# Kernel optimization log

Measured on AMD Instinct MI355X. Metric: run time of the kernel, lower is better.

Reference implementation:

```python
import math
import jax, jax.numpy as jnp
import numpy as np

N_QUBITS = 16
BATCH = 128
N_STATE = 2 ** N_QUBITS


def cnot_ring(n_qubits):
    """Permutation equivalent to a CNOT ring (faithful copy of the torch repo's numpy code)."""
    n2 = np.array([0, 2, 3, 1])
    if n_qubits == 2:
        return n2
    evens = np.zeros(2 ** (n_qubits - 1))
    answer = n2[::2]
    for i in range(1, n_qubits - 1):
        evens[:2 ** i] = answer
        a, b = np.array_split(answer, 2)
        evens[2 ** i:2 ** i + 2 ** (i - 1)] = a + 3 * 2 ** i
        evens[2 ** i + 2 ** (i - 1):2 ** (i + 1)] = b + 2 ** i
        answer = evens[:2 ** (i + 1)]
    a, b = np.split(evens.copy() + 2 ** (n_qubits - 2), 2)
    a = np.mod(a, 2 ** (n_qubits - 1))
    b, c = np.split(b, 2)
    b = b - 2 ** (n_qubits - 1)
    odds = np.concatenate((a, b, c), axis=0)[::-1]
    output = np.zeros(2 ** n_qubits)
    output[::2] = evens
    output[1::2] = odds
    return output.astype(int)


def binary_mask(n_qubits):
    """[n, 2**n] matrix; row i is bit (n-1-i from LSB) of the column index,
    matching torch binary_matrix (dim 0 of the [2]*n tensor is the MSB)."""
    idx = jnp.arange(2 ** n_qubits, dtype=jnp.int32)
    shifts = (n_qubits - 1 - jnp.arange(n_qubits, dtype=jnp.int32))
    return ((idx[None, :] >> shifts[:, None]) & 1).astype(jnp.float32)


def wht(x):
    """Walsh-Hadamard transform over the last dim of [B, N] complex state (had_big butterfly)."""
    B, N = x.shape
    n = int(math.log2(N))
    for i in range(n):
        x = x.reshape(B, 2 ** i, 2, N >> (i + 1))
        a, b = x[:, :, 0, :], x[:, :, 1, :]
        x = jnp.stack([a + b, a - b], axis=2)
    return x.reshape(B, N) * jnp.asarray(2.0 ** (-n / 2), dtype=x.dtype)


def setup_inputs() -> dict:
    key = jax.random.key(0)
    k1, k2, k3 = jax.random.split(key, 3)
    state_re = jax.random.normal(k1, (BATCH, N_STATE), dtype=jnp.float32)
    state_im = jax.random.normal(k2, (BATCH, N_STATE), dtype=jnp.float32)
    thetas = jax.random.normal(k3, (BATCH, N_QUBITS), dtype=jnp.float32)
    cnot_p = jnp.asarray(cnot_ring(N_QUBITS), dtype=jnp.int32)
    return {"state_re": state_re, "state_im": state_im, "thetas": thetas, "cnot_p": cnot_p}


def reference(state_re, state_im, thetas, cnot_p):
    # set_state('random'): l2-normalize complex state per batch row
    norm = jnp.sqrt(jnp.sum(state_re * state_re + state_im * state_im, axis=-1, keepdims=True))
    state = (state_re + 1j * state_im) / norm  # complex64 [B, N]
    # hadamard layer (had_big WHT butterfly)
    state = wht(state)
    # RZ layer: thetas @ binary mask -> phase eigenvalues exp(-i*theta/2)
    ang = thetas @ binary_mask(N_QUBITS)  # [B, N]
    state = state * jnp.exp(-0.5j * ang)
    # CNOT ring: gather permutation over the state axis
    state = state[:, cnot_p]
    # second hadamard layer
    state = wht(state)
    # measure(): probabilities |psi|^2
    return jnp.abs(state) ** 2
```

## Files before the change

### kernel.cpp

```cpp
#include <hip/hip_runtime.h>

#define NB 128
#define NS 65536

typedef float v2f __attribute__((ext_vector_type(2)));

__device__ __forceinline__ v2f pk_fma(v2f a, v2f b, v2f c) {
  v2f d;
  asm("v_pk_fma_f32 %0, %1, %2, %3" : "=v"(d) : "v"(a), "v"(b), "v"(c));
  return d;
}
__device__ __forceinline__ v2f pk_add(v2f a, v2f b) {
  v2f d;
  asm("v_pk_add_f32 %0, %1, %2" : "=v"(d) : "v"(a), "v"(b));
  return d;
}
__device__ __forceinline__ v2f pk_mul(v2f a, v2f b) {
  v2f d;
  asm("v_pk_mul_f32 %0, %1, %2" : "=v"(d) : "v"(a), "v"(b));
  return d;
}

template <int CTRL>
__device__ __forceinline__ float dppmov(float x) {
  return __int_as_float(__builtin_amdgcn_update_dpp(
      0, __float_as_int(x), CTRL, 0xF, 0xF, false));
}
__device__ __forceinline__ float xor4mov(float x) {
  int t = __builtin_amdgcn_update_dpp(0, __float_as_int(x), 0x104, 0xF, 0x5, false);
  t = __builtin_amdgcn_update_dpp(t, __float_as_int(x), 0x114, 0xF, 0xA, false);
  return __int_as_float(t);
}

__device__ __forceinline__ void wht256p(v2f (&p)[4], int lane) {
  const v2f M1 = {-1.f, -1.f};
  {
    v2f t;
    t = p[0]; p[0] = pk_add(t, p[1]); p[1] = pk_fma(M1, p[1], t);
    t = p[2]; p[2] = pk_add(t, p[3]); p[3] = pk_fma(M1, p[3], t);
    t = p[0]; p[0] = pk_add(t, p[2]); p[2] = pk_fma(M1, p[2], t);
    t = p[1]; p[1] = pk_add(t, p[3]); p[3] = pk_fma(M1, p[3], t);
  }
  const float s1f  = (lane & 1)  ? -1.f : 1.f;
  const float s2f  = (lane & 2)  ? -1.f : 1.f;
  const float s4f  = (lane & 4)  ? -1.f : 1.f;
  const float s8f  = (lane & 8)  ? -1.f : 1.f;
  const float s16f = (lane & 16) ? -1.f : 1.f;
  const float s32f = (lane & 32) ? -1.f : 1.f;
  const v2f s1 = {s1f, s1f}, s2 = {s2f, s2f}, s4 = {s4f, s4f};
  const v2f s8 = {s8f, s8f}, s16 = {s16f, s16f}, s32 = {s32f, s32f};
#pragma unroll
  for (int q = 0; q < 4; ++q) {
    v2f m = {dppmov<0xB1>(p[q].x), dppmov<0xB1>(p[q].y)};
    p[q] = pk_fma(s1, p[q], m);
  }
#pragma unroll
  for (int q = 0; q < 4; ++q) {
    v2f m = {dppmov<0x4E>(p[q].x), dppmov<0x4E>(p[q].y)};
    p[q] = pk_fma(s2, p[q], m);
  }
#pragma unroll
  for (int q = 0; q < 4; ++q) {
    v2f m = {xor4mov(p[q].x), xor4mov(p[q].y)};
    p[q] = pk_fma(s4, p[q], m);
  }
#pragma unroll
  for (int q = 0; q < 4; ++q) {
    v2f m = {dppmov<0x128>(p[q].x), dppmov<0x128>(p[q].y)};
    p[q] = pk_fma(s8, p[q], m);
  }
#pragma unroll
  for (int q = 0; q < 4; ++q) {
    auto rre = __builtin_amdgcn_permlane16_swap(__float_as_uint(p[q].x),
                                                __float_as_uint(p[q].x), false, false);
    auto rim = __builtin_amdgcn_permlane16_swap(__float_as_uint(p[q].y),
                                                __float_as_uint(p[q].y), false, false);
    v2f lo = {__uint_as_float(rre[0]), __uint_as_float(rim[0])};
    v2f hi = {__uint_as_float(rre[1]), __uint_as_float(rim[1])};
    p[q] = pk_fma(s16, hi, lo);
  }
#pragma unroll
  for (int q = 0; q < 4; ++q) {
    auto rre = __builtin_amdgcn_permlane32_swap(__float_as_uint(p[q].x),
                                                __float_as_uint(p[q].x), false, false);
    auto rim = __builtin_amdgcn_permlane32_swap(__float_as_uint(p[q].y),
                                                __float_as_uint(p[q].y), false, false);
    v2f lo = {__uint_as_float(rre[0]), __uint_as_float(rim[0])};
    v2f hi = {__uint_as_float(rre[1]), __uint_as_float(rim[1])};
    p[q] = pk_fma(s32, hi, lo);
  }
}

__global__ __launch_bounds__(1024, 8) void k1_ahi(const float* __restrict__ sre,
                                                  const float* __restrict__ sim,
                                                  const float* __restrict__ thetas,
                                                  float* __restrict__ T,
                                                  float* __restrict__ partial) {
  __shared__ float sr[32][260];
  __shared__ float si[32][260];
  __shared__ float2 phh4[64];
  __shared__ float2 phHQ[4];
  __shared__ float red[16];
  const int bid = blockIdx.x;
  const int b = bid >> 3, tile = bid & 7;
  const int lo0 = tile * 32;
  const int tid = threadIdx.x, lane = tid & 63, w = tid >> 6;
  if (tid < 64) {
    const float* tb = thetas + b * 16;
    float a = 0.f;
#pragma unroll
    for (int i = 0; i < 6; ++i)
      if ((tid >> (5 - i)) & 1) a += tb[i];
    phh4[tid] = make_float2(cosf(0.5f * a), -sinf(0.5f * a));
    if (tid < 4) {
      float aq = 0.f;
      if (tid & 1) aq += tb[7];
      if (tid & 2) aq += tb[6];
      phHQ[tid] = make_float2(cosf(0.5f * aq), -sinf(0.5f * aq));
    }
  }
  const float* pre = sre + ((size_t)b << 16);
  const float* pim = sim + ((size_t)b << 16);
  const int c = tid & 7, jr = tid >> 3;
  const int j0 = jr, j1 = jr + 128;
  const float4 vr0 = *reinterpret_cast<const float4*>(pre + j0 * 256 + lo0 + c * 4);
  const float4 vi0 = *reinterpret_cast<const float4*>(pim + j0 * 256 + lo0 + c * 4);
  const float4 vr1 = *reinterpret_cast<const float4*>(pre + j1 * 256 + lo0 + c * 4);
  const float4 vi1 = *reinterpret_cast<const float4*>(pim + j1 * 256 + lo0 + c * 4);
  float acc = vr0.x*vr0.x + vr0.y*vr0.y + vr0.z*vr0.z + vr0.w*vr0.w
            + vi0.x*vi0.x + vi0.y*vi0.y + vi0.z*vi0.z + vi0.w*vi0.w
            + vr1.x*vr1.x + vr1.y*vr1.y + vr1.z*vr1.z + vr1.w*vr1.w
            + vi1.x*vi1.x + vi1.y*vi1.y + vi1.z*vi1.z + vi1.w*vi1.w;
  {
    const int fs = ((c >> 1) & 3) << 2;
    const int j0s = j0 ^ fs, j1s = j1 ^ fs;
    sr[c*4+0][j0s] = vr0.x; sr[c*4+1][j0s] = vr0.y; sr[c*4+2][j0s] = vr0.z; sr[c*4+3][j0s] = vr0.w;
    si[c*4+0][j0s] = vi0.x; si[c*4+1][j0s] = vi0.y; si[c*4+2][j0s] = vi0.z; si[c*4+3][j0s] = vi0.w;
    sr[c*4+0][j1s] = vr1.x; sr[c*4+1][j1s] = vr1.y; sr[c*4+2][j1s] = vr1.z; sr[c*4+3][j1s] = vr1.w;
    si[c*4+0][j1s] = vi1.x; si[c*4+1][j1s] = vi1.y; si[c*4+2][j1s] = vi1.z; si[c*4+3][j1s] = vi1.w;
  }
#pragma unroll
  for (int m = 32; m >= 1; m >>= 1) acc += __shfl_xor(acc, m, 64);
  if (lane == 0) red[w] = acc;
  __syncthreads();
  if (tid == 0) {
    float sm = 0.f;
#pragma unroll
    for (int k = 0; k < 16; ++k) sm += red[k];
    partial[bid] = sm;
  }
  const float2 p4 = phh4[lane];
  float prq[4], piq[4];
#pragma unroll
  for (int q = 0; q < 4; ++q) {
    const float2 pq = phHQ[q];
    prq[q] = p4.x * pq.x - p4.y * pq.y;
    piq[q] = p4.x * pq.y + p4.y * pq.x;
  }
#pragma unroll
  for (int r = 0; r < 2; ++r) {
    const int ll = w * 2 + r;
    const int blk = lane ^ ((ll >> 3) & 3);
    const float4 a4 = *reinterpret_cast<const float4*>(&sr[ll][blk * 4]);
    const float4 b4 = *reinterpret_cast<const float4*>(&si[ll][blk * 4]);
    v2f p[4] = {{a4.x, b4.x}, {a4.y, b4.y}, {a4.z, b4.z}, {a4.w, b4.w}};
    wht256p(p, lane);
#pragma unroll
    for (int q = 0; q < 4; ++q) {
      const float ur = p[q].x, ui = p[q].y;
      const v2f t = pk_mul(p[q], (v2f){prq[q], prq[q]});
      p[q].x = fmaf(-piq[q], ui, t.x);
      p[q].y = fmaf(piq[q], ur, t.y);
    }
    wht256p(p, lane);
    *reinterpret_cast<float4*>(&sr[ll][blk * 4]) =
        make_float4(p[0].x, p[1].x, p[2].x, p[3].x);
    *reinterpret_cast<float4*>(&si[ll][blk * 4]) =
        make_float4(p[0].y, p[1].y, p[2].y, p[3].y);
  }
  __syncthreads();
  float* Tb = T + ((size_t)b << 17);
  const int m = tid >> 2, sub = tid & 3;
  float* dst = Tb + ((size_t)m << 9) + (size_t)lo0 * 2;
#pragma unroll
  for (int j = 0; j < 4; ++j) {
    const int l0 = 8 * j + 2 * sub;
    const int ms = m ^ ((j & 3) << 2);
    *reinterpret_cast<float4*>(dst + l0 * 2) =
        make_float4(sr[l0][ms], si[l0][ms], sr[l0 + 1][ms], si[l0 + 1][ms]);
  }
}

__global__ __launch_bounds__(256, 8) void k2_alo_scatter(const float* __restrict__ T,
                                                         const float* __restrict__ thetas,
                                                         const int* __restrict__ cnot,
                                                         const float* __restrict__ partial,
                                                         float* __restrict__ outp) {
  __shared__ float2 phl4[64];
  __shared__ float2 phLQ[4];
  __shared__ int sloL[64];
  __shared__ int tj[16];
  __shared__ int srow16[16];
  __shared__ float th[16];
  __shared__ float shinv;
  const int bid = blockIdx.x;
  const int x = bid & 7, s2i = bid >> 3;
  const int b = x * 16 + (s2i >> 4), tile = s2i & 15;
  const int tid = threadIdx.x, lane = tid & 63, w = tid >> 6;
  if (tid < 16) {
    th[tid] = thetas[b * 16 + tid];
    int v = 0;
#pragma unroll
    for (int i = 0; i < 16; ++i) v |= ((cnot[1 << i] >> tid) & 1) << i;
    tj[tid] = v;
  }
  if (tid == 0) {
    float sum = 0.f;
#pragma unroll
    for (int k = 0; k < 8; ++k) sum += partial[b * 8 + k];
    shinv = 1.0f / (sum * 4294967296.0f);
  }
  __syncthreads();
  if (tid < 64) {
    float a = 0.f;
#pragma unroll
    for (int i = 0; i < 6; ++i)
      if ((tid >> (5 - i)) & 1) a += th[8 + i];
    phl4[tid] = make_float2(cosf(0.5f * a), -sinf(0.5f * a));
    int v = 0;
#pragma unroll
    for (int bb = 0; bb < 6; ++bb)
      if ((tid >> bb) & 1) v ^= tj[2 + bb];
    sloL[tid] = v;
    if (tid < 4) {
      float aq = 0.f;
      if (tid & 1) aq += th[15];
      if (tid & 2) aq += th[14];
      phLQ[tid] = make_float2(cosf(0.5f * aq), -sinf(0.5f * aq));
    }
  }
  if (tid < 16) {
    const int mh = tile * 16 + tid;
    int v = 0;
#pragma unroll
    for (int bb = 0; bb < 8; ++bb)
      if ((mh >> bb) & 1) v ^= tj[8 + bb];
    srow16[tid] = v;
  }
  __syncthreads();
  const float* Tb = T + ((size_t)b << 17);
  float* ob = outp + ((size_t)b << 16);
  const float iv = shinv;
  const float2 p4 = phl4[lane];
  const int sL = sloL[lane];
  const int sq1 = tj[0], sq2 = tj[1], sq3 = tj[0] ^ tj[1];
  float prq[4], piq[4];
#pragma unroll
  for (int q = 0; q < 4; ++q) {
    const float2 pq = phLQ[q];
    prq[q] = p4.x * pq.x - p4.y * pq.y;
    piq[q] = p4.x * pq.y + p4.y * pq.x;
  }
#pragma unroll
  for (int r = 0; r < 4; ++r) {
    const int rl = w * 4 + r;
    const int mh = tile * 16 + rl;
    const float4 va = *reinterpret_cast<const float4*>(Tb + ((size_t)mh << 9) + lane * 8);
    const float4 vb = *reinterpret_cast<const float4*>(Tb + ((size_t)mh << 9) + lane * 8 + 4);
    v2f p[4] = {{va.x, va.y}, {va.z, va.w}, {vb.x, vb.y}, {vb.z, vb.w}};
    wht256p(p, lane);
#pragma unroll
    for (int q = 0; q < 4; ++q) {
      const float ur = p[q].x, ui = p[q].y;
      const v2f t = pk_mul(p[q], (v2f){prq[q], prq[q]});
      p[q].x = fmaf(-piq[q], ui, t.x);
      p[q].y = fmaf(piq[q], ur, t.y);
    }
    wht256p(p, lane);
    const int base = srow16[rl] ^ sL;
    const v2f m0 = pk_mul(p[0], p[0]);
    const v2f m1 = pk_mul(p[1], p[1]);
    const v2f m2 = pk_mul(p[2], p[2]);
    const v2f m3 = pk_mul(p[3], p[3]);
    ob[base]       = (m0.x + m0.y) * iv;
    ob[base ^ sq1] = (m1.x + m1.y) * iv;
    ob[base ^ sq2] = (m2.x + m2.y) * iv;
    ob[base ^ sq3] = (m3.x + m3.y) * iv;
  }
}

extern "C" void kernel_launch(void* const* d_in, const int* in_sizes, int n_in,
                              void* d_out, int out_size, void* d_ws, size_t ws_size,
                              hipStream_t stream) {
  const float* sre = (const float*)d_in[0];
  const float* sim = (const float*)d_in[1];
  const float* thetas = (const float*)d_in[2];
  const int* cnot = (const int*)d_in[3];
  float* outp = (float*)d_out;
  char* w = (char*)d_ws;
  const size_t CPLANE = (size_t)NB * NS * 2 * sizeof(float);
  if (ws_size < CPLANE + 8192) return;
  float* T = (float*)(w);
  float* partial = (float*)(w + CPLANE);

  hipLaunchKernelGGL(k1_ahi, dim3(1024), dim3(1024), 0, stream, sre, sim, thetas, T, partial);
  hipLaunchKernelGGL(k2_alo_scatter, dim3(2048), dim3(256), 0, stream, T, thetas, cnot, partial, outp);
}
```

Measured before the change: 61.75 us.

## Fuse both passes into one kernel with per-batch atomic counter barrier

Merges the two kernels into a single launch of 512 blocks, four per batch row. Each block runs the first WHT/phase/WHT pass over two column tiles, publishes its partial norm, then spins on a per-batch atomic counter until all four blocks of that row have finished. It then runs the second pass and the CNOT scatter on its quarter of the rows. The aim is to drop the inter-kernel launch gap and let the intermediate buffer be read back while it is likely still in cache. The cost is an extra memset launch, less parallelism in the first pass, and a deadlock risk if the blocks of one batch are not all resident at the same time.

```diff
diff --git a/kernel.cpp b/kernel.cpp
--- a/kernel.cpp
+++ b/kernel.cpp
@@ -91,180 +91,166 @@
   }
 }
 
-__global__ __launch_bounds__(1024, 8) void k1_ahi(const float* __restrict__ sre,
-                                                  const float* __restrict__ sim,
-                                                  const float* __restrict__ thetas,
-                                                  float* __restrict__ T,
-                                                  float* __restrict__ partial) {
+__global__ __launch_bounds__(1024, 8) void fused_qsim(const float* __restrict__ sre,
+                                                      const float* __restrict__ sim,
+                                                      const float* __restrict__ thetas,
+                                                      const int* __restrict__ cnot,
+                                                      float* __restrict__ T,
+                                                      float* __restrict__ partial,
+                                                      int* __restrict__ cnt,
+                                                      float* __restrict__ outp) {
   __shared__ float sr[32][260];
   __shared__ float si[32][260];
   __shared__ float2 phh4[64];
   __shared__ float2 phHQ[4];
+  __shared__ float2 phl4[64];
+  __shared__ float2 phLQ[4];
+  __shared__ int sloL[64];
+  __shared__ int tjs[16];
   __shared__ float red[16];
-  const int bid = blockIdx.x;
-  const int b = bid >> 3, tile = bid & 7;
-  const int lo0 = tile * 32;
+  __shared__ float ivs;
+  const int g = blockIdx.x;
+  const int b = g >> 2, qd = g & 3;
   const int tid = threadIdx.x, lane = tid & 63, w = tid >> 6;
-  if (tid < 64) {
-    const float* tb = thetas + b * 16;
-    float a = 0.f;
-#pragma unroll
-    for (int i = 0; i < 6; ++i)
-      if ((tid >> (5 - i)) & 1) a += tb[i];
-    phh4[tid] = make_float2(cosf(0.5f * a), -sinf(0.5f * a));
-    if (tid < 4) {
-      float aq = 0.f;
-      if (tid & 1) aq += tb[7];
-      if (tid & 2) aq += tb[6];
-      phHQ[tid] = make_float2(cosf(0.5f * aq), -sinf(0.5f * aq));
-    }
-  }
   const float* pre = sre + ((size_t)b << 16);
   const float* pim = sim + ((size_t)b << 16);
+  float* Tb = T + ((size_t)b << 17);
+  const float* tb = thetas + b * 16;
+
+  if (tid < 16) {
+    int v = 0;
+#pragma unroll
+    for (int i = 0; i < 16; ++i) v |= ((cnot[1 << i] >> tid) & 1) << i;
+    tjs[tid] = v;
+  }
+  if (tid < 64) {
+    float a = 0.f, al = 0.f;
+#pragma unroll
+    for (int i = 0; i < 6; ++i)
+      if ((tid >> (5 - i)) & 1) { a += tb[i]; al += tb[8 + i]; }
+    phh4[tid] = make_float2(cosf(0.5f * a), -sinf(0.5f * a));
+    phl4[tid] = make_float2(cosf(0.5f * al), -sinf(0.5f * al));
+    if (tid < 4) {
+      float aq = 0.f, aql = 0.f;
+      if (tid & 1) { aq += tb[7]; aql += tb[15]; }
+      if (tid & 2) { aq += tb[6]; aql += tb[14]; }
+      phHQ[tid] = make_float2(cosf(0.5f * aq), -sinf(0.5f * aq));
+      phLQ[tid] = make_float2(cosf(0.5f * aql), -sinf(0.5f * aql));
+    }
+  }
+
+  float accn = 0.f;
   const int c = tid & 7, jr = tid >> 3;
-  const int j0 = jr, j1 = jr + 128;
-  const float4 vr0 = *reinterpret_cast<const float4*>(pre + j0 * 256 + lo0 + c * 4);
-  const float4 vi0 = *reinterpret_cast<const float4*>(pim + j0 * 256 + lo0 + c * 4);
-  const float4 vr1 = *reinterpret_cast<const float4*>(pre + j1 * 256 + lo0 + c * 4);
-  const float4 vi1 = *reinterpret_cast<const float4*>(pim + j1 * 256 + lo0 + c * 4);
-  float acc = vr0.x*vr0.x + vr0.y*vr0.y + vr0.z*vr0.z + vr0.w*vr0.w
-            + vi0.x*vi0.x + vi0.y*vi0.y + vi0.z*vi0.z + vi0.w*vi0.w
-            + vr1.x*vr1.x + vr1.y*vr1.y + vr1.z*vr1.z + vr1.w*vr1.w
-            + vi1.x*vi1.x + vi1.y*vi1.y + vi1.z*vi1.z + vi1.w*vi1.w;
-  {
-    const int fs = ((c >> 1) & 3) << 2;
-    const int j0s = j0 ^ fs, j1s = j1 ^ fs;
-    sr[c*4+0][j0s] = vr0.x; sr[c*4+1][j0s] = vr0.y; sr[c*4+2][j0s] = vr0.z; sr[c*4+3][j0s] = vr0.w;
-    si[c*4+0][j0s] = vi0.x; si[c*4+1][j0s] = vi0.y; si[c*4+2][j0s] = vi0.z; si[c*4+3][j0s] = vi0.w;
-    sr[c*4+0][j1s] = vr1.x; sr[c*4+1][j1s] = vr1.y; sr[c*4+2][j1s] = vr1.z; sr[c*4+3][j1s] = vr1.w;
-    si[c*4+0][j1s] = vi1.x; si[c*4+1][j1s] = vi1.y; si[c*4+2][j1s] = vi1.z; si[c*4+3][j1s] = vi1.w;
-  }
-#pragma unroll
-  for (int m = 32; m >= 1; m >>= 1) acc += __shfl_xor(acc, m, 64);
-  if (lane == 0) red[w] = acc;
+  float prqA[4], piqA[4];
+#pragma unroll
+  for (int t = 0; t < 2; ++t) {
+    const int lo0 = (qd * 2 + t) * 32;
+    const int j0 = jr, j1 = jr + 128;
+    const float4 vr0 = *reinterpret_cast<const float4*>(pre + j0 * 256 + lo0 + c * 4);
+    const float4 vi0 = *reinterpret_cast<const float4*>(pim + j0 * 256 + lo0 + c * 4);
+    const float4 vr1 = *reinterpret_cast<const float4*>(pre + j1 * 256 + lo0 + c * 4);
+    const float4 vi1 = *reinterpret_cast<const float4*>(pim + j1 * 256 + lo0 + c * 4);
+    accn += vr0.x*vr0.x + vr0.y*vr0.y + vr0.z*vr0.z + vr0.w*vr0.w
+          + vi0.x*vi0.x + vi0.y*vi0.y + vi0.z*vi0.z + vi0.w*vi0.w
+          + vr1.x*vr1.x + vr1.y*vr1.y + vr1.z*vr1.z + vr1.w*vr1.w
+          + vi1.x*vi1.x + vi1.y*vi1.y + vi1.z*vi1.z + vi1.w*vi1.w;
+    {
+      const int fs = ((c >> 1) & 3) << 2;
+      const int j0s = j0 ^ fs, j1s = j1 ^ fs;
+      sr[c*4+0][j0s] = vr0.x; sr[c*4+1][j0s] = vr0.y; sr[c*4+2][j0s] = vr0.z; sr[c*4+3][j0s] = vr0.w;
+      si[c*4+0][j0s] = vi0.x; si[c*4+1][j0s] = vi0.y; si[c*4+2][j0s] = vi0.z; si[c*4+3][j0s] = vi0.w;
+      sr[c*4+0][j1s] = vr1.x; sr[c*4+1][j1s] = vr1.y; sr[c*4+2][j1s] = vr1.z; sr[c*4+3][j1s] = vr1.w;
+      si[c*4+0][j1s] = vi1.x; si[c*4+1][j1s] = vi1.y; si[c*4+2][j1s] = vi1.z; si[c*4+3][j1s] = vi1.w;
+    }
+    __syncthreads();
+    if (t == 0) {
+      const float2 p4 = phh4[lane];
+#pragma unroll
+      for (int q = 0; q < 4; ++q) {
+        const float2 pq = phHQ[q];
+        prqA[q] = p4.x * pq.x - p4.y * pq.y;
+        piqA[q] = p4.x * pq.y + p4.y * pq.x;
+      }
+      if (tid < 64) {
+        int v = 0;
+#pragma unroll
+        for (int bb = 0; bb < 6; ++bb)
+          if ((tid >> bb) & 1) v ^= tjs[2 + bb];
+        sloL[tid] = v;
+      }
+    }
+#pragma unroll
+    for (int r = 0; r < 2; ++r) {
+      const int ll = w * 2 + r;
+      const int blk = lane ^ ((ll >> 3) & 3);
+      const float4 a4 = *reinterpret_cast<const float4*>(&sr[ll][blk * 4]);
+      const float4 b4 = *reinterpret_cast<const float4*>(&si[ll][blk * 4]);
+      v2f p[4] = {{a4.x, b4.x}, {a4.y, b4.y}, {a4.z, b4.z}, {a4.w, b4.w}};
+      wht256p(p, lane);
+#pragma unroll
+      for (int q = 0; q < 4; ++q) {
+        const float ur = p[q].x, ui = p[q].y;
+        const v2f tt = pk_mul(p[q], (v2f){prqA[q], prqA[q]});
+        p[q].x = fmaf(-piqA[q], ui, tt.x);
+        p[q].y = fmaf(piqA[q], ur, tt.y);
+      }
+      wht256p(p, lane);
+      *reinterpret_cast<float4*>(&sr[ll][blk * 4]) =
+          make_float4(p[0].x, p[1].x, p[2].x, p[3].x);
+      *reinterpret_cast<float4*>(&si[ll][blk * 4]) =
+          make_float4(p[0].y, p[1].y, p[2].y, p[3].y);
+    }
+    __syncthreads();
+    const int m = tid >> 2, sub = tid & 3;
+    float* dst = Tb + ((size_t)m << 9) + (size_t)lo0 * 2;
+#pragma unroll
+    for (int j = 0; j < 4; ++j) {
+      const int l0 = 8 * j + 2 * sub;
+      const int ms = m ^ ((j & 3) << 2);
+      *reinterpret_cast<float4*>(dst + l0 * 2) =
+          make_float4(sr[l0][ms], si[l0][ms], sr[l0 + 1][ms], si[l0 + 1][ms]);
+    }
+    __syncthreads();
+  }
+#pragma unroll
+  for (int m2 = 32; m2 >= 1; m2 >>= 1) accn += __shfl_xor(accn, m2, 64);
+  if (lane == 0) red[w] = accn;
   __syncthreads();
   if (tid == 0) {
     float sm = 0.f;
 #pragma unroll
     for (int k = 0; k < 16; ++k) sm += red[k];
-    partial[bid] = sm;
-  }
-  const float2 p4 = phh4[lane];
+    partial[g] = sm;
+    __threadfence();
+    __hip_atomic_fetch_add(&cnt[b], 1, __ATOMIC_RELEASE, __HIP_MEMORY_SCOPE_AGENT);
+  }
+  if (tid == 0) {
+    while (__hip_atomic_load(&cnt[b], __ATOMIC_ACQUIRE, __HIP_MEMORY_SCOPE_AGENT) < 4)
+      __builtin_amdgcn_s_sleep(8);
+    const float s = partial[b * 4 + 0] + partial[b * 4 + 1] +
+                    partial[b * 4 + 2] + partial[b * 4 + 3];
+    ivs = 1.0f / (s * 4294967296.0f);
+  }
+  __syncthreads();
+  const float iv = ivs;
+  const float2 p4l = phl4[lane];
+  const int sL = sloL[lane];
+  const int sq1 = tjs[0], sq2 = tjs[1], sq3 = tjs[0] ^ tjs[1];
   float prq[4], piq[4];
 #pragma unroll
   for (int q = 0; q < 4; ++q) {
-    const float2 pq = phHQ[q];
-    prq[q] = p4.x * pq.x - p4.y * pq.y;
-    piq[q] = p4.x * pq.y + p4.y * pq.x;
-  }
-#pragma unroll
-  for (int r = 0; r < 2; ++r) {
-    const int ll = w * 2 + r;
-    const int blk = lane ^ ((ll >> 3) & 3);
-    const float4 a4 = *reinterpret_cast<const float4*>(&sr[ll][blk * 4]);
-    const float4 b4 = *reinterpret_cast<const float4*>(&si[ll][blk * 4]);
-    v2f p[4] = {{a4.x, b4.x}, {a4.y, b4.y}, {a4.z, b4.z}, {a4.w, b4.w}};
-    wht256p(p, lane);
-#pragma unroll
-    for (int q = 0; q < 4; ++q) {
-      const float ur = p[q].x, ui = p[q].y;
-      const v2f t = pk_mul(p[q], (v2f){prq[q], prq[q]});
-      p[q].x = fmaf(-piq[q], ui, t.x);
-      p[q].y = fmaf(piq[q], ur, t.y);
-    }
-    wht256p(p, lane);
-    *reinterpret_cast<float4*>(&sr[ll][blk * 4]) =
-        make_float4(p[0].x, p[1].x, p[2].x, p[3].x);
-    *reinterpret_cast<float4*>(&si[ll][blk * 4]) =
-        make_float4(p[0].y, p[1].y, p[2].y, p[3].y);
-  }
-  __syncthreads();
-  float* Tb = T + ((size_t)b << 17);
-  const int m = tid >> 2, sub = tid & 3;
-  float* dst = Tb + ((size_t)m << 9) + (size_t)lo0 * 2;
-#pragma unroll
-  for (int j = 0; j < 4; ++j) {
-    const int l0 = 8 * j + 2 * sub;
-    const int ms = m ^ ((j & 3) << 2);
-    *reinterpret_cast<float4*>(dst + l0 * 2) =
-        make_float4(sr[l0][ms], si[l0][ms], sr[l0 + 1][ms], si[l0 + 1][ms]);
-  }
-}
-
-__global__ __launch_bounds__(256, 8) void k2_alo_scatter(const float* __restrict__ T,
-                                                         const float* __restrict__ thetas,
-                                                         const int* __restrict__ cnot,
-                                                         const float* __restrict__ partial,
-                                                         float* __restrict__ outp) {
-  __shared__ float2 phl4[64];
-  __shared__ float2 phLQ[4];
-  __shared__ int sloL[64];
-  __shared__ int tj[16];
-  __shared__ int srow16[16];
-  __shared__ float th[16];
-  __shared__ float shinv;
-  const int bid = blockIdx.x;
-  const int x = bid & 7, s2i = bid >> 3;
-  const int b = x * 16 + (s2i >> 4), tile = s2i & 15;
-  const int tid = threadIdx.x, lane = tid & 63, w = tid >> 6;
-  if (tid < 16) {
-    th[tid] = thetas[b * 16 + tid];
-    int v = 0;
-#pragma unroll
-    for (int i = 0; i < 16; ++i) v |= ((cnot[1 << i] >> tid) & 1) << i;
-    tj[tid] = v;
-  }
-  if (tid == 0) {
-    float sum = 0.f;
-#pragma unroll
-    for (int k = 0; k < 8; ++k) sum += partial[b * 8 + k];
-    shinv = 1.0f / (sum * 4294967296.0f);
-  }
-  __syncthreads();
-  if (tid < 64) {
-    float a = 0.f;
-#pragma unroll
-    for (int i = 0; i < 6; ++i)
-      if ((tid >> (5 - i)) & 1) a += th[8 + i];
-    phl4[tid] = make_float2(cosf(0.5f * a), -sinf(0.5f * a));
-    int v = 0;
-#pragma unroll
-    for (int bb = 0; bb < 6; ++bb)
-      if ((tid >> bb) & 1) v ^= tj[2 + bb];
-    sloL[tid] = v;
-    if (tid < 4) {
-      float aq = 0.f;
-      if (tid & 1) aq += th[15];
-      if (tid & 2) aq += th[14];
-      phLQ[tid] = make_float2(cosf(0.5f * aq), -sinf(0.5f * aq));
-    }
-  }
-  if (tid < 16) {
-    const int mh = tile * 16 + tid;
-    int v = 0;
+    const float2 pq = phLQ[q];
+    prq[q] = p4l.x * pq.x - p4l.y * pq.y;
+    piq[q] = p4l.x * pq.y + p4l.y * pq.x;
+  }
+  float* ob = outp + ((size_t)b << 16);
+#pragma unroll
+  for (int r = 0; r < 4; ++r) {
+    const int mh = qd * 64 + w * 4 + r;
+    int srow = 0;
 #pragma unroll
     for (int bb = 0; bb < 8; ++bb)
-      if ((mh >> bb) & 1) v ^= tj[8 + bb];
-    srow16[tid] = v;
-  }
-  __syncthreads();
-  const float* Tb = T + ((size_t)b << 17);
-  float* ob = outp + ((size_t)b << 16);
-  const float iv = shinv;
-  const float2 p4 = phl4[lane];
-  const int sL = sloL[lane];
-  const int sq1 = tj[0], sq2 = tj[1], sq3 = tj[0] ^ tj[1];
-  float prq[4], piq[4];
-#pragma unroll
-  for (int q = 0; q < 4; ++q) {
-    const float2 pq = phLQ[q];
-    prq[q] = p4.x * pq.x - p4.y * pq.y;
-    piq[q] = p4.x * pq.y + p4.y * pq.x;
-  }
-#pragma unroll
-  for (int r = 0; r < 4; ++r) {
-    const int rl = w * 4 + r;
-    const int mh = tile * 16 + rl;
+      if ((mh >> bb) & 1) srow ^= tjs[8 + bb];
     const float4 va = *reinterpret_cast<const float4*>(Tb + ((size_t)mh << 9) + lane * 8);
     const float4 vb = *reinterpret_cast<const float4*>(Tb + ((size_t)mh << 9) + lane * 8 + 4);
     v2f p[4] = {{va.x, va.y}, {va.z, va.w}, {vb.x, vb.y}, {vb.z, vb.w}};
@@ -272,12 +258,12 @@
 #pragma unroll
     for (int q = 0; q < 4; ++q) {
       const float ur = p[q].x, ui = p[q].y;
-      const v2f t = pk_mul(p[q], (v2f){prq[q], prq[q]});
-      p[q].x = fmaf(-piq[q], ui, t.x);
-      p[q].y = fmaf(piq[q], ur, t.y);
+      const v2f tt = pk_mul(p[q], (v2f){prq[q], prq[q]});
+      p[q].x = fmaf(-piq[q], ui, tt.x);
+      p[q].y = fmaf(piq[q], ur, tt.y);
     }
     wht256p(p, lane);
-    const int base = srow16[rl] ^ sL;
+    const int base = srow ^ sL;
     const v2f m0 = pk_mul(p[0], p[0]);
     const v2f m1 = pk_mul(p[1], p[1]);
     const v2f m2 = pk_mul(p[2], p[2]);
@@ -302,7 +288,9 @@
   if (ws_size < CPLANE + 8192) return;
   float* T = (float*)(w);
   float* partial = (float*)(w + CPLANE);
-
-  hipLaunchKernelGGL(k1_ahi, dim3(1024), dim3(1024), 0, stream, sre, sim, thetas, T, partial);
-  hipLaunchKernelGGL(k2_alo_scatter, dim3(2048), dim3(256), 0, stream, T, thetas, cnot, partial, outp);
-}
+  int* cnt = (int*)(w + CPLANE + 2048);
+
+  hipMemsetAsync(cnt, 0, NB * sizeof(int), stream);
+  hipLaunchKernelGGL(fused_qsim, dim3(512), dim3(1024), 0, stream,
+                     sre, sim, thetas, cnot, T, partial, cnt, outp);
+}
```

New measurement: 127.0 us. +105.7%, slower.

## Process two column tiles per block in k1 and prefetch rows in k2

Applied to the files above, without the earlier changes.

k1 now handles two 32-column tiles per block, halving its grid. All global loads for both tiles are issued up front, so the second tile's data is in flight while the first is transformed. The norm reduction uses packed FMAs, and k2 reads 4 partials instead of 8. k2 loads its four rows ahead of processing them to hide memory latency. The cost is higher register pressure and extra barriers in k1, and a half-size grid that may underfill the GPU.

```diff
diff --git a/kernel.cpp b/kernel.cpp
--- a/kernel.cpp
+++ b/kernel.cpp
@@ -102,9 +102,21 @@
   __shared__ float2 phHQ[4];
   __shared__ float red[16];
   const int bid = blockIdx.x;
-  const int b = bid >> 3, tile = bid & 7;
-  const int lo0 = tile * 32;
+  const int b = bid >> 2, qd = bid & 3;
+  const int lo0 = qd * 64, lo1 = lo0 + 32;
   const int tid = threadIdx.x, lane = tid & 63, w = tid >> 6;
+  const float* pre = sre + ((size_t)b << 16);
+  const float* pim = sim + ((size_t)b << 16);
+  const int c = tid & 7, jr = tid >> 3;
+  const int j0 = jr, j1 = jr + 128;
+  const float4 vr0 = *reinterpret_cast<const float4*>(pre + j0 * 256 + lo0 + c * 4);
+  const float4 vi0 = *reinterpret_cast<const float4*>(pim + j0 * 256 + lo0 + c * 4);
+  const float4 vr1 = *reinterpret_cast<const float4*>(pre + j1 * 256 + lo0 + c * 4);
+  const float4 vi1 = *reinterpret_cast<const float4*>(pim + j1 * 256 + lo0 + c * 4);
+  const float4 wr0 = *reinterpret_cast<const float4*>(pre + j0 * 256 + lo1 + c * 4);
+  const float4 wi0 = *reinterpret_cast<const float4*>(pim + j0 * 256 + lo1 + c * 4);
+  const float4 wr1 = *reinterpret_cast<const float4*>(pre + j1 * 256 + lo1 + c * 4);
+  const float4 wi1 = *reinterpret_cast<const float4*>(pim + j1 * 256 + lo1 + c * 4);
   if (tid < 64) {
     const float* tb = thetas + b * 16;
     float a = 0.f;
@@ -119,29 +131,23 @@
       phHQ[tid] = make_float2(cosf(0.5f * aq), -sinf(0.5f * aq));
     }
   }
-  const float* pre = sre + ((size_t)b << 16);
-  const float* pim = sim + ((size_t)b << 16);
-  const int c = tid & 7, jr = tid >> 3;
-  const int j0 = jr, j1 = jr + 128;
-  const float4 vr0 = *reinterpret_cast<const float4*>(pre + j0 * 256 + lo0 + c * 4);
-  const float4 vi0 = *reinterpret_cast<const float4*>(pim + j0 * 256 + lo0 + c * 4);
-  const float4 vr1 = *reinterpret_cast<const float4*>(pre + j1 * 256 + lo0 + c * 4);
-  const float4 vi1 = *reinterpret_cast<const float4*>(pim + j1 * 256 + lo0 + c * 4);
-  float acc = vr0.x*vr0.x + vr0.y*vr0.y + vr0.z*vr0.z + vr0.w*vr0.w
-            + vi0.x*vi0.x + vi0.y*vi0.y + vi0.z*vi0.z + vi0.w*vi0.w
-            + vr1.x*vr1.x + vr1.y*vr1.y + vr1.z*vr1.z + vr1.w*vr1.w
-            + vi1.x*vi1.x + vi1.y*vi1.y + vi1.z*vi1.z + vi1.w*vi1.w;
-  {
-    const int fs = ((c >> 1) & 3) << 2;
-    const int j0s = j0 ^ fs, j1s = j1 ^ fs;
-    sr[c*4+0][j0s] = vr0.x; sr[c*4+1][j0s] = vr0.y; sr[c*4+2][j0s] = vr0.z; sr[c*4+3][j0s] = vr0.w;
-    si[c*4+0][j0s] = vi0.x; si[c*4+1][j0s] = vi0.y; si[c*4+2][j0s] = vi0.z; si[c*4+3][j0s] = vi0.w;
-    sr[c*4+0][j1s] = vr1.x; sr[c*4+1][j1s] = vr1.y; sr[c*4+2][j1s] = vr1.z; sr[c*4+3][j1s] = vr1.w;
-    si[c*4+0][j1s] = vi1.x; si[c*4+1][j1s] = vi1.y; si[c*4+2][j1s] = vi1.z; si[c*4+3][j1s] = vi1.w;
-  }
-#pragma unroll
-  for (int m = 32; m >= 1; m >>= 1) acc += __shfl_xor(acc, m, 64);
+  v2f acc2 = {0.f, 0.f};
+#define ACC4(f) do { \
+    v2f u0 = {f.x, f.y}, u1 = {f.z, f.w}; \
+    acc2 = pk_fma(u0, u0, acc2); acc2 = pk_fma(u1, u1, acc2); } while (0)
+  ACC4(vr0); ACC4(vi0); ACC4(vr1); ACC4(vi1);
+  ACC4(wr0); ACC4(wi0); ACC4(wr1); ACC4(wi1);
+#undef ACC4
+  float acc = acc2.x + acc2.y;
+#pragma unroll
+  for (int m2 = 32; m2 >= 1; m2 >>= 1) acc += __shfl_xor(acc, m2, 64);
   if (lane == 0) red[w] = acc;
+  const int fs = ((c >> 1) & 3) << 2;
+  const int j0s = j0 ^ fs, j1s = j1 ^ fs;
+  sr[c*4+0][j0s] = vr0.x; sr[c*4+1][j0s] = vr0.y; sr[c*4+2][j0s] = vr0.z; sr[c*4+3][j0s] = vr0.w;
+  si[c*4+0][j0s] = vi0.x; si[c*4+1][j0s] = vi0.y; si[c*4+2][j0s] = vi0.z; si[c*4+3][j0s] = vi0.w;
+  sr[c*4+0][j1s] = vr1.x; sr[c*4+1][j1s] = vr1.y; sr[c*4+2][j1s] = vr1.z; sr[c*4+3][j1s] = vr1.w;
+  si[c*4+0][j1s] = vi1.x; si[c*4+1][j1s] = vi1.y; si[c*4+2][j1s] = vi1.z; si[c*4+3][j1s] = vi1.w;
   __syncthreads();
   if (tid == 0) {
     float sm = 0.f;
@@ -157,37 +163,48 @@
     prq[q] = p4.x * pq.x - p4.y * pq.y;
     piq[q] = p4.x * pq.y + p4.y * pq.x;
   }
-#pragma unroll
-  for (int r = 0; r < 2; ++r) {
-    const int ll = w * 2 + r;
-    const int blk = lane ^ ((ll >> 3) & 3);
-    const float4 a4 = *reinterpret_cast<const float4*>(&sr[ll][blk * 4]);
-    const float4 b4 = *reinterpret_cast<const float4*>(&si[ll][blk * 4]);
-    v2f p[4] = {{a4.x, b4.x}, {a4.y, b4.y}, {a4.z, b4.z}, {a4.w, b4.w}};
-    wht256p(p, lane);
-#pragma unroll
-    for (int q = 0; q < 4; ++q) {
-      const float ur = p[q].x, ui = p[q].y;
-      const v2f t = pk_mul(p[q], (v2f){prq[q], prq[q]});
-      p[q].x = fmaf(-piq[q], ui, t.x);
-      p[q].y = fmaf(piq[q], ur, t.y);
-    }
-    wht256p(p, lane);
-    *reinterpret_cast<float4*>(&sr[ll][blk * 4]) =
-        make_float4(p[0].x, p[1].x, p[2].x, p[3].x);
-    *reinterpret_cast<float4*>(&si[ll][blk * 4]) =
-        make_float4(p[0].y, p[1].y, p[2].y, p[3].y);
-  }
-  __syncthreads();
   float* Tb = T + ((size_t)b << 17);
-  const int m = tid >> 2, sub = tid & 3;
-  float* dst = Tb + ((size_t)m << 9) + (size_t)lo0 * 2;
-#pragma unroll
-  for (int j = 0; j < 4; ++j) {
-    const int l0 = 8 * j + 2 * sub;
-    const int ms = m ^ ((j & 3) << 2);
-    *reinterpret_cast<float4*>(dst + l0 * 2) =
-        make_float4(sr[l0][ms], si[l0][ms], sr[l0 + 1][ms], si[l0 + 1][ms]);
+  const int mrow = tid >> 2, sub = tid & 3;
+#pragma unroll
+  for (int t = 0; t < 2; ++t) {
+#pragma unroll
+    for (int r = 0; r < 2; ++r) {
+      const int ll = w * 2 + r;
+      const int blk = lane ^ ((ll >> 3) & 3);
+      const float4 a4 = *reinterpret_cast<const float4*>(&sr[ll][blk * 4]);
+      const float4 b4 = *reinterpret_cast<const float4*>(&si[ll][blk * 4]);
+      v2f p[4] = {{a4.x, b4.x}, {a4.y, b4.y}, {a4.z, b4.z}, {a4.w, b4.w}};
+      wht256p(p, lane);
+#pragma unroll
+      for (int q = 0; q < 4; ++q) {
+        const float ur = p[q].x, ui = p[q].y;
+        const v2f tt = pk_mul(p[q], (v2f){prq[q], prq[q]});
+        p[q].x = fmaf(-piq[q], ui, tt.x);
+        p[q].y = fmaf(piq[q], ur, tt.y);
+      }
+      wht256p(p, lane);
+      *reinterpret_cast<float4*>(&sr[ll][blk * 4]) =
+          make_float4(p[0].x, p[1].x, p[2].x, p[3].x);
+      *reinterpret_cast<float4*>(&si[ll][blk * 4]) =
+          make_float4(p[0].y, p[1].y, p[2].y, p[3].y);
+    }
+    __syncthreads();
+    float* dst = Tb + ((size_t)mrow << 9) + (size_t)(t == 0 ? lo0 : lo1) * 2;
+#pragma unroll
+    for (int j = 0; j < 4; ++j) {
+      const int l0 = 8 * j + 2 * sub;
+      const int ms = mrow ^ ((j & 3) << 2);
+      *reinterpret_cast<float4*>(dst + l0 * 2) =
+          make_float4(sr[l0][ms], si[l0][ms], sr[l0 + 1][ms], si[l0 + 1][ms]);
+    }
+    if (t == 0) {
+      __syncthreads();
+      sr[c*4+0][j0s] = wr0.x; sr[c*4+1][j0s] = wr0.y; sr[c*4+2][j0s] = wr0.z; sr[c*4+3][j0s] = wr0.w;
+      si[c*4+0][j0s] = wi0.x; si[c*4+1][j0s] = wi0.y; si[c*4+2][j0s] = wi0.z; si[c*4+3][j0s] = wi0.w;
+      sr[c*4+0][j1s] = wr1.x; sr[c*4+1][j1s] = wr1.y; sr[c*4+2][j1s] = wr1.z; sr[c*4+3][j1s] = wr1.w;
+      si[c*4+0][j1s] = wi1.x; si[c*4+1][j1s] = wi1.y; si[c*4+2][j1s] = wi1.z; si[c*4+3][j1s] = wi1.w;
+      __syncthreads();
+    }
   }
 }
 
@@ -217,7 +234,7 @@
   if (tid == 0) {
     float sum = 0.f;
 #pragma unroll
-    for (int k = 0; k < 8; ++k) sum += partial[b * 8 + k];
+    for (int k = 0; k < 4; ++k) sum += partial[b * 4 + k];
     shinv = 1.0f / (sum * 4294967296.0f);
   }
   __syncthreads();
@@ -261,32 +278,40 @@
     prq[q] = p4.x * pq.x - p4.y * pq.y;
     piq[q] = p4.x * pq.y + p4.y * pq.x;
   }
-#pragma unroll
-  for (int r = 0; r < 4; ++r) {
-    const int rl = w * 4 + r;
-    const int mh = tile * 16 + rl;
-    const float4 va = *reinterpret_cast<const float4*>(Tb + ((size_t)mh << 9) + lane * 8);
-    const float4 vb = *reinterpret_cast<const float4*>(Tb + ((size_t)mh << 9) + lane * 8 + 4);
-    v2f p[4] = {{va.x, va.y}, {va.z, va.w}, {vb.x, vb.y}, {vb.z, vb.w}};
-    wht256p(p, lane);
-#pragma unroll
-    for (int q = 0; q < 4; ++q) {
-      const float ur = p[q].x, ui = p[q].y;
-      const v2f t = pk_mul(p[q], (v2f){prq[q], prq[q]});
-      p[q].x = fmaf(-piq[q], ui, t.x);
-      p[q].y = fmaf(piq[q], ur, t.y);
-    }
-    wht256p(p, lane);
-    const int base = srow16[rl] ^ sL;
-    const v2f m0 = pk_mul(p[0], p[0]);
-    const v2f m1 = pk_mul(p[1], p[1]);
-    const v2f m2 = pk_mul(p[2], p[2]);
-    const v2f m3 = pk_mul(p[3], p[3]);
-    ob[base]       = (m0.x + m0.y) * iv;
-    ob[base ^ sq1] = (m1.x + m1.y) * iv;
-    ob[base ^ sq2] = (m2.x + m2.y) * iv;
-    ob[base ^ sq3] = (m3.x + m3.y) * iv;
-  }
+  const float* rbase = Tb + ((size_t)(tile * 16 + w * 4) << 9) + lane * 8;
+#define LDROW(A, B, r) \
+  const float4 A = *reinterpret_cast<const float4*>(rbase + (r) * 512); \
+  const float4 B = *reinterpret_cast<const float4*>(rbase + (r) * 512 + 4)
+#define PROC(A, B, r) do { \
+    v2f p[4] = {{A.x, A.y}, {A.z, A.w}, {B.x, B.y}, {B.z, B.w}}; \
+    wht256p(p, lane); \
+    _Pragma("unroll") \
+    for (int q = 0; q < 4; ++q) { \
+      const float ur = p[q].x, ui = p[q].y; \
+      const v2f tt = pk_mul(p[q], (v2f){prq[q], prq[q]}); \
+      p[q].x = fmaf(-piq[q], ui, tt.x); \
+      p[q].y = fmaf(piq[q], ur, tt.y); \
+    } \
+    wht256p(p, lane); \
+    const int base = srow16[w * 4 + (r)] ^ sL; \
+    const v2f m0 = pk_mul(p[0], p[0]); \
+    const v2f m1 = pk_mul(p[1], p[1]); \
+    const v2f m2 = pk_mul(p[2], p[2]); \
+    const v2f m3 = pk_mul(p[3], p[3]); \
+    ob[base]       = (m0.x + m0.y) * iv; \
+    ob[base ^ sq1] = (m1.x + m1.y) * iv; \
+    ob[base ^ sq2] = (m2.x + m2.y) * iv; \
+    ob[base ^ sq3] = (m3.x + m3.y) * iv; } while (0)
+  LDROW(A0, B0, 0);
+  LDROW(A1, B1, 1);
+  LDROW(A2, B2, 2);
+  PROC(A0, B0, 0);
+  LDROW(A3, B3, 3);
+  PROC(A1, B1, 1);
+  PROC(A2, B2, 2);
+  PROC(A3, B3, 3);
+#undef LDROW
+#undef PROC
 }
 
 extern "C" void kernel_launch(void* const* d_in, const int* in_sizes, int n_in,
@@ -303,6 +328,6 @@
   float* T = (float*)(w);
   float* partial = (float*)(w + CPLANE);
 
-  hipLaunchKernelGGL(k1_ahi, dim3(1024), dim3(1024), 0, stream, sre, sim, thetas, T, partial);
+  hipLaunchKernelGGL(k1_ahi, dim3(512), dim3(1024), 0, stream, sre, sim, thetas, T, partial);
   hipLaunchKernelGGL(k2_alo_scatter, dim3(2048), dim3(256), 0, stream, T, thetas, cnot, partial, outp);
 }
```

New measurement: 70.66 us. 14.4% more time.
